# Kernel tuning notes

Measured on AMD Instinct MI355X. Metric: run time of the kernel, lower is better.

## Reference

```python
import jax, jax.numpy as jnp
import numpy as np

L_Q, B, Q = 512, 256, 512
IN, H, A = 512, 1024, 512
L_H = 512


def _xavier(key, shape):
    fan_out, fan_in = shape
    lim = (6.0 / (fan_in + fan_out)) ** 0.5
    return jax.random.uniform(key, shape, minval=-lim, maxval=lim, dtype=jnp.float32)


def setup_inputs() -> dict:
    key = jax.random.key(0)
    ks = jax.random.split(key, 12)
    return {
        "query_data": jax.random.normal(ks[0], (L_Q, B, Q), dtype=jnp.float32),
        "query_mask": jnp.ones((L_Q, B), dtype=jnp.float32),
        "input": jax.random.normal(ks[1], (B, IN), dtype=jnp.float32),
        "parent_index": jax.random.randint(ks[2], (B,), 0, L_H),
        "history": jax.random.normal(ks[3], (L_H, B, H), dtype=jnp.float32),
        "h0": jax.random.normal(ks[4], (B, H), dtype=jnp.float32),
        "c0": jax.random.normal(ks[5], (B, H), dtype=jnp.float32),
        "W_ih": _xavier(ks[6], (4 * H, IN + Q + H)),
        "W_hh": _xavier(ks[7], (4 * H, H)),
        "b_ih": jnp.zeros((4 * H,), dtype=jnp.float32),
        "b_hh": jnp.zeros((4 * H,), dtype=jnp.float32),
        "att1_w": _xavier(ks[8], (A, Q + H)),
        "att1_b": jnp.zeros((A,), dtype=jnp.float32),
        "att2_w": _xavier(ks[9], (1, A)),
        "att2_b": jnp.zeros((1,), dtype=jnp.float32),
    }


def reference(query_data, query_mask, input, parent_index, history, h0, c0,
              W_ih, W_hh, b_ih, b_hh, att1_w, att1_b, att2_w, att2_b):
    L_q, Bn, _ = query_data.shape
    # attention: concat broadcast h0 with query, two linears + tanh
    h_ctx = jnp.broadcast_to(h0[None], (L_q, Bn, h0.shape[1]))
    att = jnp.concatenate([h_ctx, query_data], axis=2)          # (L_q, B, H+Q)
    att_hidden = jnp.tanh(att @ att1_w.T + att1_b)               # (L_q, B, A)
    att_raw = (att_hidden @ att2_w.T + att2_b)[..., 0]           # (L_q, B)
    # manual masked softmax over L_q (faithful: max taken before masking)
    e = jnp.exp(att_raw - jnp.max(att_raw, axis=0, keepdims=True)) * query_mask
    w = e / jnp.sum(e, axis=0, keepdims=True)                    # (L_q, B)
    ctx_vec = jnp.sum(query_data * w[..., None], axis=0)         # (B, Q)
    # query_history: gather instead of one-hot matmul
    h_parent = history[parent_index, jnp.arange(Bn)]             # (B, H)
    # LSTMCell (dropout=0 -> identity); torch gate order i, f, g, o
    x = jnp.concatenate([input, ctx_vec, h_parent], axis=1)      # (B, IN+Q+H)
    gates = x @ W_ih.T + b_ih + h0 @ W_hh.T + b_hh               # (B, 4H)
    i, f, g, o = jnp.split(gates, 4, axis=1)
    c1 = jax.nn.sigmoid(f) * c0 + jax.nn.sigmoid(i) * jnp.tanh(g)
    h1 = jax.nn.sigmoid(o) * jnp.tanh(c1)
    return ctx_vec, h1, c1
```

## Files before the change

### kernel.cpp

```cpp
#include <hip/hip_runtime.h>
#include <hip/hip_bf16.h>


typedef short bf16x8 __attribute__((ext_vector_type(8)));
typedef float f32x4 __attribute__((ext_vector_type(4)));
typedef unsigned short u16x4 __attribute__((ext_vector_type(4)));

__device__ __forceinline__ unsigned short f2bf(float f) {
  unsigned int u = __builtin_bit_cast(unsigned int, f);
  u += 0x7fffu + ((u >> 16) & 1u);
  return (unsigned short)(u >> 16);
}
__device__ __forceinline__ float bf2f(unsigned short u) {
  unsigned int x = (unsigned int)u << 16;
  return __builtin_bit_cast(float, x);
}
__device__ __forceinline__ float fast_tanh(float x) {
  float e = __expf(2.0f * x);
  return 1.0f - 2.0f / (e + 1.0f);
}
__device__ __forceinline__ float fast_sig(float x) {
  return 1.0f / (1.0f + __expf(-x));
}
__device__ __forceinline__ f32x4 mfma16(bf16x8 a, bf16x8 b, f32x4 c) {
  return __builtin_amdgcn_mfma_f32_16x16x32_bf16(a, b, c, 0, 0, 0);
}

__global__ void k_prep(const float* __restrict__ a1w, const float* __restrict__ h0,
                       unsigned short* __restrict__ wqf, float* __restrict__ part1) {
  __shared__ float sh[4096], swt[4096];
  int bx = blockIdx.x;
  if (bx < 128) {
    int g = bx * 256 + threadIdx.x;
    int lane = g & 63, frag = g >> 6;
    int ab = frag >> 4, ksf = frag & 15;
    int a = ab * 16 + (lane & 15);
    int k = ksf * 32 + (lane >> 4) * 8;
    const float* src = a1w + (size_t)a * 1536 + 1024 + k;
    float4 v0 = *reinterpret_cast<const float4*>(src);
    float4 v1 = *reinterpret_cast<const float4*>(src + 4);
    unsigned short* dst = wqf + ((size_t)frag * 64 + lane) * 8;
    *(u16x4*)dst       = u16x4{ f2bf(v0.x), f2bf(v0.y), f2bf(v0.z), f2bf(v0.w) };
    *(u16x4*)(dst + 4) = u16x4{ f2bf(v1.x), f2bf(v1.y), f2bf(v1.z), f2bf(v1.w) };
    return;
  }
  int blk = bx - 128;
  int at = blk & 7, bt = (blk >> 3) & 3, ksp = blk >> 5;
  int a0 = at * 64, b0 = bt * 64, kbase = ksp * 128;
  int t = threadIdx.x;
  int ta = t & 15, tb = t >> 4;
  float acc[4][4] = {};
  for (int half = 0; half < 2; half++) {
    int k0 = kbase + half * 64;
    for (int i = 0; i < 4; i++) {
      int u = i * 256 + t;
      int row = u >> 4, c4 = (u & 15) << 2;
      float4 vh = *reinterpret_cast<const float4*>(h0 + (size_t)(b0 + row) * 1024 + k0 + c4);
      float4 vw = *reinterpret_cast<const float4*>(a1w + (size_t)(a0 + row) * 1536 + k0 + c4);
      int off = (row * 256 + c4 * 4) ^ ((row & 7) << 4);
      *(float4*)((char*)sh + off) = vh;
      *(float4*)((char*)swt + off) = vw;
    }
    __syncthreads();
    for (int k4 = 0; k4 < 16; k4++) {
      float4 hv[4], wv[4];
#pragma unroll
      for (int i = 0; i < 4; i++) {
        int rh = tb + 16 * i;
        hv[i] = *(const float4*)((char*)sh + ((rh * 256 + k4 * 16) ^ ((rh & 7) << 4)));
        int ra = ta + 16 * i;
        wv[i] = *(const float4*)((char*)swt + ((ra * 256 + k4 * 16) ^ ((ra & 7) << 4)));
      }
#pragma unroll
      for (int i = 0; i < 4; i++)
#pragma unroll
        for (int j = 0; j < 4; j++)
          acc[i][j] += hv[i].x * wv[j].x + hv[i].y * wv[j].y +
                       hv[i].z * wv[j].z + hv[i].w * wv[j].w;
    }
    __syncthreads();
  }
  float* dst = part1 + (size_t)ksp * 131072;
#pragma unroll
  for (int i = 0; i < 4; i++)
#pragma unroll
    for (int j = 0; j < 4; j++)
      dst[(size_t)(b0 + tb + 16 * i) * 512 + a0 + ta + 16 * j] = acc[i][j];
}

__global__ void k_base2(const float* __restrict__ part1, const float* __restrict__ a1b,
                        float* __restrict__ base) {
  int idx = blockIdx.x * 256 + threadIdx.x;
  float s = a1b[idx & 511];
  for (int ks = 0; ks < 8; ks++) s += part1[(size_t)ks * 131072 + idx];
  base[idx] = s;
}

__global__ __launch_bounds__(256, 2) void k_attgemm(
    const float* __restrict__ qd, const unsigned short* __restrict__ wqf,
    const float* __restrict__ base, const float* __restrict__ w2,
    float* __restrict__ araw, unsigned short* __restrict__ qbf) {
  extern __shared__ char smem[];
  int t = threadIdx.x;
  int m0 = blockIdx.x * 64;
  for (int i = 0; i < 32; i++) {
    int u = i * 256 + t;
    int row = u >> 7, c4 = (u & 127) << 2;
    float4 v = *reinterpret_cast<const float4*>(qd + (size_t)(m0 + row) * 512 + c4);
    int off = (row * 1024 + c4 * 2) ^ ((row & 7) << 4);
    u16x4 bv = u16x4{ f2bf(v.x), f2bf(v.y), f2bf(v.z), f2bf(v.w) };
    *(u16x4*)(smem + off) = bv;
    *(u16x4*)((char*)qbf + (size_t)m0 * 1024 + off) = bv;
  }
  __syncthreads();
  int lane = t & 63, lr = lane & 15, lh = lane >> 4;
  int w = t >> 6;
  int b0 = m0 & 255;
  float rs[4][4] = {};
  for (int chunk = 0; chunk < 2; chunk++) {
    f32x4 acc[4][4] = {};
    int colbase = chunk * 256 + w * 64;
#pragma unroll 4
    for (int ks = 0; ks < 16; ks++) {
      bf16x8 aF[4], bF[4];
#pragma unroll
      for (int mi = 0; mi < 4; mi++) {
        int row = mi * 16 + lr;
        int off = (row * 1024 + (ks * 32 + lh * 8) * 2) ^ ((row & 7) << 4);
        aF[mi] = *(const bf16x8*)(smem + off);
      }
#pragma unroll
      for (int ni = 0; ni < 4; ni++) {
        int ab = (colbase >> 4) + ni;
        bF[ni] = *(const bf16x8*)(wqf + ((size_t)(ab * 16 + ks) * 64 + lane) * 8);
      }
#pragma unroll
      for (int mi = 0; mi < 4; mi++)
#pragma unroll
        for (int ni = 0; ni < 4; ni++)
          acc[mi][ni] = mfma16(aF[mi], bF[ni], acc[mi][ni]);
    }
#pragma unroll
    for (int ni = 0; ni < 4; ni++) {
      int a = colbase + ni * 16 + lr;
      float w2v = w2[a];
#pragma unroll
      for (int mi = 0; mi < 4; mi++)
#pragma unroll
        for (int r = 0; r < 4; r++) {
          int row = mi * 16 + lh * 4 + r;
          float val = acc[mi][ni][r] + base[(size_t)(b0 + row) * 512 + a];
          rs[mi][r] += fast_tanh(val) * w2v;
        }
    }
  }
#pragma unroll
  for (int mi = 0; mi < 4; mi++)
#pragma unroll
    for (int r = 0; r < 4; r++) {
      float v = rs[mi][r];
      v += __shfl_xor(v, 1); v += __shfl_xor(v, 2);
      v += __shfl_xor(v, 4); v += __shfl_xor(v, 8);
      rs[mi][r] = v;
    }
  __syncthreads();
  float* sRed = (float*)smem;
  if (lr == 0)
#pragma unroll
    for (int mi = 0; mi < 4; mi++)
#pragma unroll
      for (int r = 0; r < 4; r++)
        sRed[w * 64 + mi * 16 + lh * 4 + r] = rs[mi][r];
  __syncthreads();
  if (t < 64) {
    float v = sRed[t] + sRed[64 + t] + sRed[128 + t] + sRed[192 + t];
    int m = m0 + t;
    araw[(size_t)(m & 255) * 512 + (m >> 8)] = v;
  }
}

__global__ __launch_bounds__(256, 4) void k_ctx(
    const unsigned short* __restrict__ qbf, const float* __restrict__ araw,
    const float* __restrict__ mask, float* __restrict__ out) {
  __shared__ float sw[512];
  __shared__ float red[8];
  __shared__ float sRed[4][512];
  int b = blockIdx.x, t = threadIdx.x;
  float x0 = araw[b * 512 + t];
  float x1 = araw[b * 512 + t + 256];
  float mx = fmaxf(x0, x1);
#pragma unroll
  for (int off = 1; off < 64; off <<= 1) mx = fmaxf(mx, __shfl_xor(mx, off));
  int wv = t >> 6, ln = t & 63;
  if (ln == 0) red[wv] = mx;
  __syncthreads();
  mx = fmaxf(fmaxf(red[0], red[1]), fmaxf(red[2], red[3]));
  float e0 = __expf(x0 - mx) * mask[(size_t)t * 256 + b];
  float e1 = __expf(x1 - mx) * mask[(size_t)(t + 256) * 256 + b];
  float s = e0 + e1;
#pragma unroll
  for (int off = 1; off < 64; off <<= 1) s += __shfl_xor(s, off);
  if (ln == 0) red[4 + wv] = s;
  __syncthreads();
  s = red[4] + red[5] + red[6] + red[7];
  float inv = 1.0f / s;
  sw[t] = e0 * inv;
  sw[t + 256] = e1 * inv;
  __syncthreads();
  int qc = t & 63, ls = t >> 6;
  const char* basep = (const char*)qbf + (size_t)b * 1024 + ((size_t)(qc ^ (b & 7)) << 4);
  float acc[8] = {};
#pragma unroll 8
  for (int i = 0; i < 128; i++) {
    int l = ls * 128 + i;
    uint4 v = *(const uint4*)(basep + (size_t)l * 262144);
    float wl = sw[l];
    acc[0] += wl * bf2f((unsigned short)(v.x & 0xffff));
    acc[1] += wl * bf2f((unsigned short)(v.x >> 16));
    acc[2] += wl * bf2f((unsigned short)(v.y & 0xffff));
    acc[3] += wl * bf2f((unsigned short)(v.y >> 16));
    acc[4] += wl * bf2f((unsigned short)(v.z & 0xffff));
    acc[5] += wl * bf2f((unsigned short)(v.z >> 16));
    acc[6] += wl * bf2f((unsigned short)(v.w & 0xffff));
    acc[7] += wl * bf2f((unsigned short)(v.w >> 16));
  }
#pragma unroll
  for (int j = 0; j < 8; j++) sRed[ls][qc * 8 + j] = acc[j];
  __syncthreads();
  for (int q = t; q < 512; q += 256)
    out[b * 512 + q] = sRed[0][q] + sRed[1][q] + sRed[2][q] + sRed[3][q];
}

__global__ void k_xf(const float* __restrict__ inp, const float* __restrict__ ctx,
                     const float* __restrict__ hist, const int* __restrict__ pidx,
                     const float* __restrict__ h0, unsigned short* __restrict__ xf) {
  int g = blockIdx.x * 256 + threadIdx.x;
  int lane = g & 63, frag = g >> 6;
  int mb = frag / 96, kstep = frag % 96;
  int b = mb * 16 + (lane & 15);
  int k = kstep * 32 + (lane >> 4) * 8;
  const float* src;
  if (k < 512)       src = inp  + (size_t)b * 512 + k;
  else if (k < 1024) src = ctx  + (size_t)b * 512 + (k - 512);
  else if (k < 2048) src = hist + ((size_t)pidx[b] * 256 + b) * 1024 + (k - 1024);
  else               src = h0   + (size_t)b * 1024 + (k - 2048);
  float4 v0 = *reinterpret_cast<const float4*>(src);
  float4 v1 = *reinterpret_cast<const float4*>(src + 4);
  unsigned short* dst = xf + ((size_t)frag * 64 + lane) * 8;
  *(u16x4*)dst       = u16x4{ f2bf(v0.x), f2bf(v0.y), f2bf(v0.z), f2bf(v0.w) };
  *(u16x4*)(dst + 4) = u16x4{ f2bf(v1.x), f2bf(v1.y), f2bf(v1.z), f2bf(v1.w) };
}

__global__ __launch_bounds__(256, 2) void k_gates(
    const unsigned short* __restrict__ xf, const float* __restrict__ Wih,
    const float* __restrict__ Whh, float* __restrict__ part) {
  int blk = blockIdx.x;
  int nt = blk & 63, ksp = blk >> 6;
  int n0 = nt * 64, kbeg = ksp * 768;
  int t = threadIdx.x;
  int lane = t & 63, lr = lane & 15, lh = lane >> 4;
  int w = t >> 6;
  f32x4 acc[4][4] = {};
#pragma unroll 2
  for (int ks = 0; ks < 24; ks++) {
    int k0 = kbeg + ks * 32;
    int kstep = k0 >> 5;
    bf16x8 aF[4], bF[4];
#pragma unroll
    for (int mi = 0; mi < 4; mi++) {
      int mb = w * 4 + mi;
      aF[mi] = *(const bf16x8*)(xf + ((size_t)(mb * 96 + kstep) * 64 + lane) * 8);
    }
    const float* Wp; int ldw, kk;
    if (k0 < 2048) { Wp = Wih; ldw = 2048; kk = k0; }
    else           { Wp = Whh; ldw = 1024; kk = k0 - 2048; }
#pragma unroll
    for (int ni = 0; ni < 4; ni++) {
      int j = n0 + ni * 16 + lr;
      const float* src = Wp + (size_t)j * ldw + kk + lh * 8;
      float4 v0 = *reinterpret_cast<const float4*>(src);
      float4 v1 = *reinterpret_cast<const float4*>(src + 4);
      bf16x8 bv;
      bv[0] = (short)f2bf(v0.x); bv[1] = (short)f2bf(v0.y);
      bv[2] = (short)f2bf(v0.z); bv[3] = (short)f2bf(v0.w);
      bv[4] = (short)f2bf(v1.x); bv[5] = (short)f2bf(v1.y);
      bv[6] = (short)f2bf(v1.z); bv[7] = (short)f2bf(v1.w);
      bF[ni] = bv;
    }
#pragma unroll
    for (int mi = 0; mi < 4; mi++)
#pragma unroll
      for (int ni = 0; ni < 4; ni++)
        acc[mi][ni] = mfma16(aF[mi], bF[ni], acc[mi][ni]);
  }
  float* dst = part + (size_t)ksp * (256 * 4096);
#pragma unroll
  for (int mi = 0; mi < 4; mi++)
#pragma unroll
    for (int ni = 0; ni < 4; ni++)
#pragma unroll
      for (int r = 0; r < 4; r++) {
        int b = w * 64 + mi * 16 + lh * 4 + r;
        int j = n0 + ni * 16 + lr;
        dst[(size_t)b * 4096 + j] = acc[mi][ni][r];
      }
}

__global__ void k_lstm(const float* __restrict__ part, const float* __restrict__ bih,
                       const float* __restrict__ bhh, const float* __restrict__ c0,
                       float* __restrict__ out) {
  int idx = blockIdx.x * 256 + threadIdx.x;
  int h = idx & 1023;
  int b = idx >> 10;
  const float* p = part + (size_t)b * 4096;
  float gi = bih[h] + bhh[h];
  float gf = bih[1024 + h] + bhh[1024 + h];
  float gg = bih[2048 + h] + bhh[2048 + h];
  float go = bih[3072 + h] + bhh[3072 + h];
#pragma unroll
  for (int ks = 0; ks < 4; ks++) {
    const float* q = p + (size_t)ks * 1048576;
    gi += q[h]; gf += q[1024 + h]; gg += q[2048 + h]; go += q[3072 + h];
  }
  float c = fast_sig(gf) * c0[idx] + fast_sig(gi) * fast_tanh(gg);
  float hv = fast_sig(go) * fast_tanh(c);
  out[131072 + idx] = hv;
  out[393216 + idx] = c;
}

extern "C" void kernel_launch(void* const* d_in, const int* in_sizes, int n_in,
                              void* d_out, int out_size, void* d_ws, size_t ws_size,
                              hipStream_t stream) {
  const float* qd    = (const float*)d_in[0];
  const float* qmask = (const float*)d_in[1];
  const float* inp   = (const float*)d_in[2];
  const int*   pidx  = (const int*)d_in[3];
  const float* hist  = (const float*)d_in[4];
  const float* h0    = (const float*)d_in[5];
  const float* c0    = (const float*)d_in[6];
  const float* Wih   = (const float*)d_in[7];
  const float* Whh   = (const float*)d_in[8];
  const float* bih   = (const float*)d_in[9];
  const float* bhh   = (const float*)d_in[10];
  const float* a1w   = (const float*)d_in[11];
  const float* a1b   = (const float*)d_in[12];
  const float* a2w   = (const float*)d_in[13];
  float* outF = (float*)d_out;

  char* ws = (char*)d_ws;
  unsigned short* wqf  = (unsigned short*)(ws);
  float*          base = (float*)(ws + 524288);
  float*          araw = (float*)(ws + 1048576);
  unsigned short* xf   = (unsigned short*)(ws + 2097152);
  float*          p1   = (float*)(ws + 3670016);
  float*          pg   = (float*)(ws + 7864320);
  unsigned short* qbf  = (unsigned short*)(ws + 33554432);

  (void)hipFuncSetAttribute((const void*)k_attgemm,
                            hipFuncAttributeMaxDynamicSharedMemorySize, 65536);

  k_prep   <<<384,  256, 0, stream>>>(a1w, h0, wqf, p1);
  k_base2  <<<512,  256, 0, stream>>>(p1, a1b, base);
  k_attgemm<<<2048, 256, 65536, stream>>>(qd, wqf, base, a2w, araw, qbf);
  k_ctx    <<<256,  256, 0, stream>>>(qbf, araw, qmask, outF);
  k_xf     <<<384,  256, 0, stream>>>(inp, outF, hist, pidx, h0, xf);
  k_gates  <<<256,  256, 0, stream>>>(xf, Wih, Whh, pg);
  k_lstm   <<<1024, 256, 0, stream>>>(pg, bih, bhh, c0, outF);
}
```

Baseline: 291.0 us.

## Raise parallelism in attention GEMM, context reduction and gate GEMM

The attention GEMM now uses 512 threads per block. Each warp owns one 64-column slice, and the K dimension is staged through half-size shared memory in two phases, so the LDS footprint halves and occupancy rises. The context kernel is split four ways over the sequence, with partial sums reduced inside k_xf, which also writes ctx_vec to the output. The gate GEMM uses narrower N tiles and an 8-way K split, giving 1024 blocks. The cost is more partial-sum traffic to global memory, plus an extra barrier and reload phase in the attention kernel.

New measurement: 292.5 us. Within noise of the previous version (+0.5%).

```diff
diff --git a/kernel.cpp b/kernel.cpp
--- a/kernel.cpp
+++ b/kernel.cpp
@@ -96,43 +96,45 @@
   base[idx] = s;
 }
 
-__global__ __launch_bounds__(256, 2) void k_attgemm(
+__global__ __launch_bounds__(512, 4) void k_attgemm(
     const float* __restrict__ qd, const unsigned short* __restrict__ wqf,
     const float* __restrict__ base, const float* __restrict__ w2,
     float* __restrict__ araw, unsigned short* __restrict__ qbf) {
   extern __shared__ char smem[];
   int t = threadIdx.x;
   int m0 = blockIdx.x * 64;
-  for (int i = 0; i < 32; i++) {
-    int u = i * 256 + t;
-    int row = u >> 7, c4 = (u & 127) << 2;
-    float4 v = *reinterpret_cast<const float4*>(qd + (size_t)(m0 + row) * 512 + c4);
-    int off = (row * 1024 + c4 * 2) ^ ((row & 7) << 4);
-    u16x4 bv = u16x4{ f2bf(v.x), f2bf(v.y), f2bf(v.z), f2bf(v.w) };
-    *(u16x4*)(smem + off) = bv;
-    *(u16x4*)((char*)qbf + (size_t)m0 * 1024 + off) = bv;
-  }
-  __syncthreads();
   int lane = t & 63, lr = lane & 15, lh = lane >> 4;
   int w = t >> 6;
   int b0 = m0 & 255;
-  float rs[4][4] = {};
-  for (int chunk = 0; chunk < 2; chunk++) {
-    f32x4 acc[4][4] = {};
-    int colbase = chunk * 256 + w * 64;
+  f32x4 acc[4][4] = {};
+  for (int p = 0; p < 2; p++) {
+    if (p) __syncthreads();
+    for (int i = 0; i < 8; i++) {
+      int u = i * 512 + t;
+      int row = u >> 6, cl4 = (u & 63) << 2;
+      float4 v = *reinterpret_cast<const float4*>(
+          qd + (size_t)(m0 + row) * 512 + p * 256 + cl4);
+      u16x4 bv = u16x4{ f2bf(v.x), f2bf(v.y), f2bf(v.z), f2bf(v.w) };
+      int loff = (row * 512 + cl4 * 2) ^ ((row & 7) << 4);
+      *(u16x4*)(smem + loff) = bv;
+      *(u16x4*)((char*)qbf + (size_t)(m0 + row) * 1024 + p * 512 +
+                ((cl4 * 2) ^ ((row & 7) << 4))) = bv;
+    }
+    __syncthreads();
 #pragma unroll 4
-    for (int ks = 0; ks < 16; ks++) {
+    for (int ksl = 0; ksl < 8; ksl++) {
       bf16x8 aF[4], bF[4];
 #pragma unroll
       for (int mi = 0; mi < 4; mi++) {
         int row = mi * 16 + lr;
-        int off = (row * 1024 + (ks * 32 + lh * 8) * 2) ^ ((row & 7) << 4);
+        int off = (row * 512 + (ksl * 32 + lh * 8) * 2) ^ ((row & 7) << 4);
         aF[mi] = *(const bf16x8*)(smem + off);
       }
+      int kstep = p * 8 + ksl;
 #pragma unroll
       for (int ni = 0; ni < 4; ni++) {
-        int ab = (colbase >> 4) + ni;
-        bF[ni] = *(const bf16x8*)(wqf + ((size_t)(ab * 16 + ks) * 64 + lane) * 8);
+        int ab = w * 4 + ni;
+        bF[ni] = *(const bf16x8*)(wqf + ((size_t)(ab * 16 + kstep) * 64 + lane) * 8);
       }
 #pragma unroll
       for (int mi = 0; mi < 4; mi++)
@@ -140,19 +142,20 @@
         for (int ni = 0; ni < 4; ni++)
           acc[mi][ni] = mfma16(aF[mi], bF[ni], acc[mi][ni]);
     }
-#pragma unroll
-    for (int ni = 0; ni < 4; ni++) {
-      int a = colbase + ni * 16 + lr;
-      float w2v = w2[a];
-#pragma unroll
-      for (int mi = 0; mi < 4; mi++)
-#pragma unroll
-        for (int r = 0; r < 4; r++) {
-          int row = mi * 16 + lh * 4 + r;
-          float val = acc[mi][ni][r] + base[(size_t)(b0 + row) * 512 + a];
-          rs[mi][r] += fast_tanh(val) * w2v;
-        }
-    }
+  }
+  float rs[4][4] = {};
+#pragma unroll
+  for (int ni = 0; ni < 4; ni++) {
+    int a = w * 64 + ni * 16 + lr;
+    float w2v = w2[a];
+#pragma unroll
+    for (int mi = 0; mi < 4; mi++)
+#pragma unroll
+      for (int r = 0; r < 4; r++) {
+        int row = mi * 16 + lh * 4 + r;
+        float val = acc[mi][ni][r] + base[(size_t)(b0 + row) * 512 + a];
+        rs[mi][r] += fast_tanh(val) * w2v;
+      }
   }
 #pragma unroll
   for (int mi = 0; mi < 4; mi++)
@@ -173,7 +176,9 @@
         sRed[w * 64 + mi * 16 + lh * 4 + r] = rs[mi][r];
   __syncthreads();
   if (t < 64) {
-    float v = sRed[t] + sRed[64 + t] + sRed[128 + t] + sRed[192 + t];
+    float v = 0.0f;
+#pragma unroll
+    for (int j = 0; j < 8; j++) v += sRed[j * 64 + t];
     int m = m0 + t;
     araw[(size_t)(m & 255) * 512 + (m >> 8)] = v;
   }
@@ -181,11 +186,12 @@
 
 __global__ __launch_bounds__(256, 4) void k_ctx(
     const unsigned short* __restrict__ qbf, const float* __restrict__ araw,
-    const float* __restrict__ mask, float* __restrict__ out) {
+    const float* __restrict__ mask, float* __restrict__ part) {
   __shared__ float sw[512];
   __shared__ float red[8];
   __shared__ float sRed[4][512];
-  int b = blockIdx.x, t = threadIdx.x;
+  int b = blockIdx.x >> 2, lc = blockIdx.x & 3;
+  int t = threadIdx.x;
   float x0 = araw[b * 512 + t];
   float x1 = araw[b * 512 + t + 256];
   float mx = fmaxf(x0, x1);
@@ -211,8 +217,8 @@
   const char* basep = (const char*)qbf + (size_t)b * 1024 + ((size_t)(qc ^ (b & 7)) << 4);
   float acc[8] = {};
 #pragma unroll 8
-  for (int i = 0; i < 128; i++) {
-    int l = ls * 128 + i;
+  for (int i = 0; i < 32; i++) {
+    int l = lc * 128 + ls * 32 + i;
     uint4 v = *(const uint4*)(basep + (size_t)l * 262144);
     float wl = sw[l];
     acc[0] += wl * bf2f((unsigned short)(v.x & 0xffff));
@@ -228,44 +234,61 @@
   for (int j = 0; j < 8; j++) sRed[ls][qc * 8 + j] = acc[j];
   __syncthreads();
   for (int q = t; q < 512; q += 256)
-    out[b * 512 + q] = sRed[0][q] + sRed[1][q] + sRed[2][q] + sRed[3][q];
-}
-
-__global__ void k_xf(const float* __restrict__ inp, const float* __restrict__ ctx,
+    part[((size_t)lc * 256 + b) * 512 + q] =
+        sRed[0][q] + sRed[1][q] + sRed[2][q] + sRed[3][q];
+}
+
+__global__ void k_xf(const float* __restrict__ inp, const float* __restrict__ ctxp,
                      const float* __restrict__ hist, const int* __restrict__ pidx,
-                     const float* __restrict__ h0, unsigned short* __restrict__ xf) {
+                     const float* __restrict__ h0, unsigned short* __restrict__ xf,
+                     float* __restrict__ outF) {
   int g = blockIdx.x * 256 + threadIdx.x;
   int lane = g & 63, frag = g >> 6;
   int mb = frag / 96, kstep = frag % 96;
   int b = mb * 16 + (lane & 15);
   int k = kstep * 32 + (lane >> 4) * 8;
-  const float* src;
-  if (k < 512)       src = inp  + (size_t)b * 512 + k;
-  else if (k < 1024) src = ctx  + (size_t)b * 512 + (k - 512);
-  else if (k < 2048) src = hist + ((size_t)pidx[b] * 256 + b) * 1024 + (k - 1024);
-  else               src = h0   + (size_t)b * 1024 + (k - 2048);
-  float4 v0 = *reinterpret_cast<const float4*>(src);
-  float4 v1 = *reinterpret_cast<const float4*>(src + 4);
+  float4 v0, v1;
+  if (k >= 512 && k < 1024) {
+    int q0 = k - 512;
+    v0 = float4{0, 0, 0, 0}; v1 = float4{0, 0, 0, 0};
+#pragma unroll
+    for (int lc = 0; lc < 4; lc++) {
+      const float* p = ctxp + ((size_t)lc * 256 + b) * 512 + q0;
+      float4 a0 = *reinterpret_cast<const float4*>(p);
+      float4 a1 = *reinterpret_cast<const float4*>(p + 4);
+      v0.x += a0.x; v0.y += a0.y; v0.z += a0.z; v0.w += a0.w;
+      v1.x += a1.x; v1.y += a1.y; v1.z += a1.z; v1.w += a1.w;
+    }
+    *reinterpret_cast<float4*>(outF + (size_t)b * 512 + q0) = v0;
+    *reinterpret_cast<float4*>(outF + (size_t)b * 512 + q0 + 4) = v1;
+  } else {
+    const float* src;
+    if (k < 512)       src = inp  + (size_t)b * 512 + k;
+    else if (k < 2048) src = hist + ((size_t)pidx[b] * 256 + b) * 1024 + (k - 1024);
+    else               src = h0   + (size_t)b * 1024 + (k - 2048);
+    v0 = *reinterpret_cast<const float4*>(src);
+    v1 = *reinterpret_cast<const float4*>(src + 4);
+  }
   unsigned short* dst = xf + ((size_t)frag * 64 + lane) * 8;
   *(u16x4*)dst       = u16x4{ f2bf(v0.x), f2bf(v0.y), f2bf(v0.z), f2bf(v0.w) };
   *(u16x4*)(dst + 4) = u16x4{ f2bf(v1.x), f2bf(v1.y), f2bf(v1.z), f2bf(v1.w) };
 }
 
-__global__ __launch_bounds__(256, 2) void k_gates(
+__global__ __launch_bounds__(256, 4) void k_gates(
     const unsigned short* __restrict__ xf, const float* __restrict__ Wih,
     const float* __restrict__ Whh, float* __restrict__ part) {
   int blk = blockIdx.x;
-  int nt = blk & 63, ksp = blk >> 6;
-  int n0 = nt * 64, kbeg = ksp * 768;
+  int nt = blk & 127, ksp = blk >> 7;
+  int n0 = nt * 32, kbeg = ksp * 384;
   int t = threadIdx.x;
   int lane = t & 63, lr = lane & 15, lh = lane >> 4;
   int w = t >> 6;
-  f32x4 acc[4][4] = {};
+  f32x4 acc[4][2] = {};
 #pragma unroll 2
-  for (int ks = 0; ks < 24; ks++) {
+  for (int ks = 0; ks < 12; ks++) {
     int k0 = kbeg + ks * 32;
     int kstep = k0 >> 5;
-    bf16x8 aF[4], bF[4];
+    bf16x8 aF[4], bF[2];
 #pragma unroll
     for (int mi = 0; mi < 4; mi++) {
       int mb = w * 4 + mi;
@@ -275,7 +298,7 @@
     if (k0 < 2048) { Wp = Wih; ldw = 2048; kk = k0; }
     else           { Wp = Whh; ldw = 1024; kk = k0 - 2048; }
 #pragma unroll
-    for (int ni = 0; ni < 4; ni++) {
+    for (int ni = 0; ni < 2; ni++) {
       int j = n0 + ni * 16 + lr;
       const float* src = Wp + (size_t)j * ldw + kk + lh * 8;
       float4 v0 = *reinterpret_cast<const float4*>(src);
@@ -290,14 +313,14 @@
 #pragma unroll
     for (int mi = 0; mi < 4; mi++)
 #pragma unroll
-      for (int ni = 0; ni < 4; ni++)
+      for (int ni = 0; ni < 2; ni++)
         acc[mi][ni] = mfma16(aF[mi], bF[ni], acc[mi][ni]);
   }
   float* dst = part + (size_t)ksp * (256 * 4096);
 #pragma unroll
   for (int mi = 0; mi < 4; mi++)
 #pragma unroll
-    for (int ni = 0; ni < 4; ni++)
+    for (int ni = 0; ni < 2; ni++)
 #pragma unroll
       for (int r = 0; r < 4; r++) {
         int b = w * 64 + mi * 16 + lh * 4 + r;
@@ -318,7 +341,7 @@
   float gg = bih[2048 + h] + bhh[2048 + h];
   float go = bih[3072 + h] + bhh[3072 + h];
 #pragma unroll
-  for (int ks = 0; ks < 4; ks++) {
+  for (int ks = 0; ks < 8; ks++) {
     const float* q = p + (size_t)ks * 1048576;
     gi += q[h]; gf += q[1024 + h]; gg += q[2048 + h]; go += q[3072 + h];
   }
@@ -353,17 +376,18 @@
   float*          araw = (float*)(ws + 1048576);
   unsigned short* xf   = (unsigned short*)(ws + 2097152);
   float*          p1   = (float*)(ws + 3670016);
-  float*          pg   = (float*)(ws + 7864320);
-  unsigned short* qbf  = (unsigned short*)(ws + 33554432);
+  float*          ctxp = (float*)(ws + 7864320);
+  float*          pg   = (float*)(ws + 16777216);
+  unsigned short* qbf  = (unsigned short*)(ws + 67108864);
 
   (void)hipFuncSetAttribute((const void*)k_attgemm,
-                            hipFuncAttributeMaxDynamicSharedMemorySize, 65536);
+                            hipFuncAttributeMaxDynamicSharedMemorySize, 32768);
 
   k_prep   <<<384,  256, 0, stream>>>(a1w, h0, wqf, p1);
   k_base2  <<<512,  256, 0, stream>>>(p1, a1b, base);
-  k_attgemm<<<2048, 256, 65536, stream>>>(qd, wqf, base, a2w, araw, qbf);
-  k_ctx    <<<256,  256, 0, stream>>>(qbf, araw, qmask, outF);
-  k_xf     <<<384,  256, 0, stream>>>(inp, outF, hist, pidx, h0, xf);
-  k_gates  <<<256,  256, 0, stream>>>(xf, Wih, Whh, pg);
+  k_attgemm<<<2048, 512, 32768, stream>>>(qd, wqf, base, a2w, araw, qbf);
+  k_ctx    <<<1024, 256, 0, stream>>>(qbf, araw, qmask, ctxp);
+  k_xf     <<<384,  256, 0, stream>>>(inp, ctxp, hist, pidx, h0, xf, outF);
+  k_gates  <<<1024, 256, 0, stream>>>(xf, Wih, Whh, pg);
   k_lstm   <<<1024, 256, 0, stream>>>(pg, bih, bhh, c0, outF);
 }
```

## Fuse softmax-weighted context accumulation into attention GEMM and retile gates GEMM

Applied to the files above, without the earlier changes.

The attention GEMM is restructured so that each block handles 16 batch entries across 64 query positions. Inside the same block it computes the attention scores, exponentiates them with the mask applied, and accumulates the weighted query rows straight from LDS into partial numerators and denominators. A small reduction kernel then sums these partials and divides. This removes the bf16 copy of query_data that was written to global memory and re-read by the separate context kernel. The softmax now skips max subtraction, which depends on the scores staying bounded (tanh outputs times small weights). Separately, the gates GEMM uses 32-column tiles with twice as many blocks and a higher occupancy hint.

Measured after the change: 249.6 us. 14.2% less time.

```diff
diff --git a/kernel.cpp b/kernel.cpp
--- a/kernel.cpp
+++ b/kernel.cpp
@@ -96,30 +96,34 @@
   base[idx] = s;
 }
 
-__global__ __launch_bounds__(256, 2) void k_attgemm(
+__global__ __launch_bounds__(512, 2) void k_attgemm(
     const float* __restrict__ qd, const unsigned short* __restrict__ wqf,
     const float* __restrict__ base, const float* __restrict__ w2,
-    float* __restrict__ araw, unsigned short* __restrict__ qbf) {
+    const float* __restrict__ mask, float* __restrict__ nump,
+    float* __restrict__ denp) {
   extern __shared__ char smem[];
+  float* sRed = (float*)(smem + 65536);
+  float* e_lds = (float*)(smem + 65536 + 2048);
   int t = threadIdx.x;
-  int m0 = blockIdx.x * 64;
-  for (int i = 0; i < 32; i++) {
-    int u = i * 256 + t;
-    int row = u >> 7, c4 = (u & 127) << 2;
-    float4 v = *reinterpret_cast<const float4*>(qd + (size_t)(m0 + row) * 512 + c4);
-    int off = (row * 1024 + c4 * 2) ^ ((row & 7) << 4);
-    u16x4 bv = u16x4{ f2bf(v.x), f2bf(v.y), f2bf(v.z), f2bf(v.w) };
-    *(u16x4*)(smem + off) = bv;
-    *(u16x4*)((char*)qbf + (size_t)m0 * 1024 + off) = bv;
-  }
-  __syncthreads();
+  int bt = blockIdx.x & 15, lt = blockIdx.x >> 4;
+  int b0 = bt * 16, l0 = lt * 16;
   int lane = t & 63, lr = lane & 15, lh = lane >> 4;
   int w = t >> 6;
-  int b0 = m0 & 255;
-  float rs[4][4] = {};
-  for (int chunk = 0; chunk < 2; chunk++) {
+  int b_own = t >> 5, q0 = (t & 31) * 16;
+  float ctx_acc[16] = {};
+  float den_acc = 0.0f;
+  for (int ls = 0; ls < 4; ls++) {
+    int l_base = l0 + ls * 4;
+    for (int i = 0; i < 16; i++) {
+      int u = i * 512 + t;
+      int row = u >> 7, c4 = (u & 127) << 2;
+      float4 v = *reinterpret_cast<const float4*>(
+          qd + ((size_t)(l_base + (row >> 4)) * 256 + b0 + (row & 15)) * 512 + c4);
+      int loff = (row * 1024 + c4 * 2) ^ ((row & 7) << 4);
+      *(u16x4*)(smem + loff) = u16x4{ f2bf(v.x), f2bf(v.y), f2bf(v.z), f2bf(v.w) };
+    }
+    __syncthreads();
     f32x4 acc[4][4] = {};
-    int colbase = chunk * 256 + w * 64;
 #pragma unroll 4
     for (int ks = 0; ks < 16; ks++) {
       bf16x8 aF[4], bF[4];
@@ -131,7 +135,7 @@
       }
 #pragma unroll
       for (int ni = 0; ni < 4; ni++) {
-        int ab = (colbase >> 4) + ni;
+        int ab = w * 4 + ni;
         bF[ni] = *(const bf16x8*)(wqf + ((size_t)(ab * 16 + ks) * 64 + lane) * 8);
       }
 #pragma unroll
@@ -140,95 +144,79 @@
         for (int ni = 0; ni < 4; ni++)
           acc[mi][ni] = mfma16(aF[mi], bF[ni], acc[mi][ni]);
     }
+    float rs[4][4] = {};
 #pragma unroll
     for (int ni = 0; ni < 4; ni++) {
-      int a = colbase + ni * 16 + lr;
+      int a = w * 64 + ni * 16 + lr;
       float w2v = w2[a];
 #pragma unroll
       for (int mi = 0; mi < 4; mi++)
 #pragma unroll
         for (int r = 0; r < 4; r++) {
-          int row = mi * 16 + lh * 4 + r;
-          float val = acc[mi][ni][r] + base[(size_t)(b0 + row) * 512 + a];
+          int b = b0 + lh * 4 + r;
+          float val = acc[mi][ni][r] + base[(size_t)b * 512 + a];
           rs[mi][r] += fast_tanh(val) * w2v;
         }
     }
-  }
-#pragma unroll
-  for (int mi = 0; mi < 4; mi++)
-#pragma unroll
-    for (int r = 0; r < 4; r++) {
-      float v = rs[mi][r];
-      v += __shfl_xor(v, 1); v += __shfl_xor(v, 2);
-      v += __shfl_xor(v, 4); v += __shfl_xor(v, 8);
-      rs[mi][r] = v;
-    }
-  __syncthreads();
-  float* sRed = (float*)smem;
-  if (lr == 0)
 #pragma unroll
     for (int mi = 0; mi < 4; mi++)
 #pragma unroll
-      for (int r = 0; r < 4; r++)
-        sRed[w * 64 + mi * 16 + lh * 4 + r] = rs[mi][r];
-  __syncthreads();
-  if (t < 64) {
-    float v = sRed[t] + sRed[64 + t] + sRed[128 + t] + sRed[192 + t];
-    int m = m0 + t;
-    araw[(size_t)(m & 255) * 512 + (m >> 8)] = v;
-  }
-}
-
-__global__ __launch_bounds__(256, 4) void k_ctx(
-    const unsigned short* __restrict__ qbf, const float* __restrict__ araw,
-    const float* __restrict__ mask, float* __restrict__ out) {
-  __shared__ float sw[512];
-  __shared__ float red[8];
-  __shared__ float sRed[4][512];
-  int b = blockIdx.x, t = threadIdx.x;
-  float x0 = araw[b * 512 + t];
-  float x1 = araw[b * 512 + t + 256];
-  float mx = fmaxf(x0, x1);
-#pragma unroll
-  for (int off = 1; off < 64; off <<= 1) mx = fmaxf(mx, __shfl_xor(mx, off));
-  int wv = t >> 6, ln = t & 63;
-  if (ln == 0) red[wv] = mx;
-  __syncthreads();
-  mx = fmaxf(fmaxf(red[0], red[1]), fmaxf(red[2], red[3]));
-  float e0 = __expf(x0 - mx) * mask[(size_t)t * 256 + b];
-  float e1 = __expf(x1 - mx) * mask[(size_t)(t + 256) * 256 + b];
-  float s = e0 + e1;
-#pragma unroll
-  for (int off = 1; off < 64; off <<= 1) s += __shfl_xor(s, off);
-  if (ln == 0) red[4 + wv] = s;
-  __syncthreads();
-  s = red[4] + red[5] + red[6] + red[7];
-  float inv = 1.0f / s;
-  sw[t] = e0 * inv;
-  sw[t + 256] = e1 * inv;
-  __syncthreads();
-  int qc = t & 63, ls = t >> 6;
-  const char* basep = (const char*)qbf + (size_t)b * 1024 + ((size_t)(qc ^ (b & 7)) << 4);
-  float acc[8] = {};
+      for (int r = 0; r < 4; r++) {
+        float v = rs[mi][r];
+        v += __shfl_xor(v, 1); v += __shfl_xor(v, 2);
+        v += __shfl_xor(v, 4); v += __shfl_xor(v, 8);
+        rs[mi][r] = v;
+      }
+    if (lr == 0)
+#pragma unroll
+      for (int mi = 0; mi < 4; mi++)
+#pragma unroll
+        for (int r = 0; r < 4; r++)
+          sRed[w * 64 + mi * 16 + lh * 4 + r] = rs[mi][r];
+    __syncthreads();
+    if (t < 64) {
+      float araw = 0.0f;
+#pragma unroll
+      for (int j = 0; j < 8; j++) araw += sRed[j * 64 + t];
+      int l = l_base + (t >> 4), b = b0 + (t & 15);
+      e_lds[t] = __expf(araw) * mask[(size_t)l * 256 + b];
+    }
+    __syncthreads();
+#pragma unroll
+    for (int li = 0; li < 4; li++) {
+      int row = li * 16 + b_own;
+      float e = e_lds[row];
+      if ((t & 31) == 0) den_acc += e;
+      int sw = (row & 7) << 4;
+      bf16x8 v0 = *(const bf16x8*)(smem + ((row * 1024 + q0 * 2) ^ sw));
+      bf16x8 v1 = *(const bf16x8*)(smem + ((row * 1024 + q0 * 2 + 16) ^ sw));
+#pragma unroll
+      for (int j = 0; j < 8; j++) {
+        ctx_acc[j]     += e * bf2f((unsigned short)v0[j]);
+        ctx_acc[8 + j] += e * bf2f((unsigned short)v1[j]);
+      }
+    }
+    __syncthreads();
+  }
+  float* dst = nump + ((size_t)lt * 256 + b0 + b_own) * 512 + q0;
+#pragma unroll
+  for (int j = 0; j < 4; j++)
+    *reinterpret_cast<float4*>(dst + j * 4) =
+        float4{ ctx_acc[j * 4], ctx_acc[j * 4 + 1], ctx_acc[j * 4 + 2], ctx_acc[j * 4 + 3] };
+  if ((t & 31) == 0) denp[lt * 256 + b0 + b_own] = den_acc;
+}
+
+__global__ void k_ctxred(const float* __restrict__ nump, const float* __restrict__ denp,
+                         float* __restrict__ outF) {
+  int idx = blockIdx.x * 256 + threadIdx.x;
+  int b = idx >> 9;
+  float s = 0.0f, d = 0.0f;
 #pragma unroll 8
-  for (int i = 0; i < 128; i++) {
-    int l = ls * 128 + i;
-    uint4 v = *(const uint4*)(basep + (size_t)l * 262144);
-    float wl = sw[l];
-    acc[0] += wl * bf2f((unsigned short)(v.x & 0xffff));
-    acc[1] += wl * bf2f((unsigned short)(v.x >> 16));
-    acc[2] += wl * bf2f((unsigned short)(v.y & 0xffff));
-    acc[3] += wl * bf2f((unsigned short)(v.y >> 16));
-    acc[4] += wl * bf2f((unsigned short)(v.z & 0xffff));
-    acc[5] += wl * bf2f((unsigned short)(v.z >> 16));
-    acc[6] += wl * bf2f((unsigned short)(v.w & 0xffff));
-    acc[7] += wl * bf2f((unsigned short)(v.w >> 16));
-  }
-#pragma unroll
-  for (int j = 0; j < 8; j++) sRed[ls][qc * 8 + j] = acc[j];
-  __syncthreads();
-  for (int q = t; q < 512; q += 256)
-    out[b * 512 + q] = sRed[0][q] + sRed[1][q] + sRed[2][q] + sRed[3][q];
+  for (int lt = 0; lt < 32; lt++) {
+    s += nump[(size_t)lt * 131072 + idx];
+    d += denp[lt * 256 + b];
+  }
+  outF[idx] = s / d;
 }
 
 __global__ void k_xf(const float* __restrict__ inp, const float* __restrict__ ctx,
@@ -251,21 +239,21 @@
   *(u16x4*)(dst + 4) = u16x4{ f2bf(v1.x), f2bf(v1.y), f2bf(v1.z), f2bf(v1.w) };
 }
 
-__global__ __launch_bounds__(256, 2) void k_gates(
+__global__ __launch_bounds__(256, 4) void k_gates(
     const unsigned short* __restrict__ xf, const float* __restrict__ Wih,
     const float* __restrict__ Whh, float* __restrict__ part) {
   int blk = blockIdx.x;
-  int nt = blk & 63, ksp = blk >> 6;
-  int n0 = nt * 64, kbeg = ksp * 768;
+  int nt = blk & 127, ksp = blk >> 7;
+  int n0 = nt * 32, kbeg = ksp * 768;
   int t = threadIdx.x;
   int lane = t & 63, lr = lane & 15, lh = lane >> 4;
   int w = t >> 6;
-  f32x4 acc[4][4] = {};
+  f32x4 acc[4][2] = {};
 #pragma unroll 2
   for (int ks = 0; ks < 24; ks++) {
     int k0 = kbeg + ks * 32;
     int kstep = k0 >> 5;
-    bf16x8 aF[4], bF[4];
+    bf16x8 aF[4], bF[2];
 #pragma unroll
     for (int mi = 0; mi < 4; mi++) {
       int mb = w * 4 + mi;
@@ -275,7 +263,7 @@
     if (k0 < 2048) { Wp = Wih; ldw = 2048; kk = k0; }
     else           { Wp = Whh; ldw = 1024; kk = k0 - 2048; }
 #pragma unroll
-    for (int ni = 0; ni < 4; ni++) {
+    for (int ni = 0; ni < 2; ni++) {
       int j = n0 + ni * 16 + lr;
       const float* src = Wp + (size_t)j * ldw + kk + lh * 8;
       float4 v0 = *reinterpret_cast<const float4*>(src);
@@ -290,14 +278,14 @@
 #pragma unroll
     for (int mi = 0; mi < 4; mi++)
 #pragma unroll
-      for (int ni = 0; ni < 4; ni++)
+      for (int ni = 0; ni < 2; ni++)
         acc[mi][ni] = mfma16(aF[mi], bF[ni], acc[mi][ni]);
   }
   float* dst = part + (size_t)ksp * (256 * 4096);
 #pragma unroll
   for (int mi = 0; mi < 4; mi++)
 #pragma unroll
-    for (int ni = 0; ni < 4; ni++)
+    for (int ni = 0; ni < 2; ni++)
 #pragma unroll
       for (int r = 0; r < 4; r++) {
         int b = w * 64 + mi * 16 + lh * 4 + r;
@@ -350,20 +338,20 @@
   char* ws = (char*)d_ws;
   unsigned short* wqf  = (unsigned short*)(ws);
   float*          base = (float*)(ws + 524288);
-  float*          araw = (float*)(ws + 1048576);
-  unsigned short* xf   = (unsigned short*)(ws + 2097152);
-  float*          p1   = (float*)(ws + 3670016);
-  float*          pg   = (float*)(ws + 7864320);
-  unsigned short* qbf  = (unsigned short*)(ws + 33554432);
+  float*          p1   = (float*)(ws + 1048576);
+  unsigned short* xf   = (unsigned short*)(ws + 5242880);
+  float*          denp = (float*)(ws + 6815744);
+  float*          nump = (float*)(ws + 8388608);
+  float*          pg   = (float*)(ws + 25165824);
 
   (void)hipFuncSetAttribute((const void*)k_attgemm,
-                            hipFuncAttributeMaxDynamicSharedMemorySize, 65536);
+                            hipFuncAttributeMaxDynamicSharedMemorySize, 67840);
 
   k_prep   <<<384,  256, 0, stream>>>(a1w, h0, wqf, p1);
   k_base2  <<<512,  256, 0, stream>>>(p1, a1b, base);
-  k_attgemm<<<2048, 256, 65536, stream>>>(qd, wqf, base, a2w, araw, qbf);
-  k_ctx    <<<256,  256, 0, stream>>>(qbf, araw, qmask, outF);
+  k_attgemm<<<512,  512, 67840, stream>>>(qd, wqf, base, a2w, qmask, nump, denp);
+  k_ctxred <<<512,  256, 0, stream>>>(nump, denp, outF);
   k_xf     <<<384,  256, 0, stream>>>(inp, outF, hist, pidx, h0, xf);
-  k_gates  <<<256,  256, 0, stream>>>(xf, Wih, Whh, pg);
+  k_gates  <<<512,  256, 0, stream>>>(xf, Wih, Whh, pg);
   k_lstm   <<<1024, 256, 0, stream>>>(pg, bih, bhh, c0, outF);
 }
```
